# Optimization experiments

Hardware: AMD Instinct MI355X
Metric: run time of the kernel (lower is better)

## Reference

```python
import jax, jax.numpy as jnp
import numpy as np

B, S = 256, 2048
VOCAB, E, H, OUT = 10, 32, 64, 10


def setup_inputs() -> dict:
    key = jax.random.key(0)
    ks = jax.random.split(key, 8)
    num1 = jax.random.randint(ks[0], (B, S), 0, VOCAB, dtype=jnp.int32)
    num2 = jax.random.randint(ks[1], (B, S), 0, VOCAB, dtype=jnp.int32)
    embed = jax.random.normal(ks[2], (VOCAB, E), dtype=jnp.float32) * 0.05
    Wx = jax.random.normal(ks[3], (2 * E, H), dtype=jnp.float32) * (1.0 / np.sqrt(2 * E))
    Wh = jax.random.normal(ks[4], (H, H), dtype=jnp.float32) * (1.0 / np.sqrt(H))
    b = jnp.zeros((H,), dtype=jnp.float32)
    Wd = jax.random.normal(ks[5], (H, OUT), dtype=jnp.float32) * (1.0 / np.sqrt(H))
    bd = jnp.zeros((OUT,), dtype=jnp.float32)
    return {"num1": num1, "num2": num2, "embed": embed, "Wx": Wx,
            "Wh": Wh, "b": b, "Wd": Wd, "bd": bd}


def reference(num1, num2, embed, Wx, Wh, b, Wd, bd):
    # embedding lookup + concat -> [B, S, 2E]
    x = jnp.concatenate([embed[num1], embed[num2]], axis=2)
    # precompute input projection once (big GEMM), scan only the recurrence
    xw = jnp.einsum('bse,eh->bsh', x, Wx) + b  # [B, S, H]

    def step(h, xw_t):
        h = jnp.tanh(xw_t + h @ Wh)  # SimpleRNNCell: tanh(x W + h U + b)
        return h, h

    h0 = jnp.zeros((x.shape[0], Wh.shape[0]), dtype=x.dtype)
    _, hs = jax.lax.scan(step, h0, jnp.swapaxes(xw, 0, 1))  # hs: [S, B, H]
    hs = jnp.swapaxes(hs, 0, 1)  # [B, S, H]
    logits = jnp.einsum('bsh,ho->bso', hs, Wd) + bd  # [B, S, 10]
    return logits
```

## Files before the change

kernel.cpp:

```cpp
#include <hip/hip_runtime.h>

namespace {
typedef float v2f __attribute__((ext_vector_type(2)));
constexpr int kB = 256;
constexpr int kS = 2048;
constexpr int kV = 10;
constexpr int kE = 32;
constexpr int kH = 64;
constexpr int kO = 10;
constexpr int kT = 16;
constexpr int kPad = 68;
constexpr int kTiles = kS / kT;
constexpr float kC = 2.885390081777927f;

__device__ __forceinline__ float step_tanh(float s) {
    s = __builtin_amdgcn_fmed3f(s, -26.f, 26.f);
    float e = __builtin_amdgcn_exp2f(s);
    float r = __builtin_amdgcn_rcpf(e + 1.f);
    return fmaf(-2.f, r, 1.f);
}

__device__ __forceinline__ void do_logits(const float* __restrict__ hb,
                                          const float (* __restrict__ WdT)[kPad],
                                          const float* __restrict__ bdL,
                                          float* __restrict__ out, int obase, int l)
{
    #pragma unroll
    for (int r = 0; r < 3; ++r) {
        int f = r * 64 + l;
        if (f < kT * kO) {
            int tl = f / kO;
            int o  = f - tl * kO;
            const float4* hb4 = reinterpret_cast<const float4*>(hb + tl * kPad);
            const float4* wd4 = reinterpret_cast<const float4*>(&WdT[o][0]);
            float a0 = bdL[o], a1 = 0.f, a2 = 0.f, a3 = 0.f;
            #pragma unroll
            for (int c = 0; c < kH / 4; ++c) {
                float4 h4 = hb4[c];
                float4 w4 = wd4[c];
                a0 = fmaf(h4.x, w4.x, a0);
                a1 = fmaf(h4.y, w4.y, a1);
                a2 = fmaf(h4.z, w4.z, a2);
                a3 = fmaf(h4.w, w4.w, a3);
            }
            out[obase + f] = (a0 + a1) + (a2 + a3);
        }
    }
}

__global__ __launch_bounds__(128, 1)
void rnn_fused(const int* __restrict__ num1, const int* __restrict__ num2,
               const float* __restrict__ embed, const float* __restrict__ Wx,
               const float* __restrict__ Wh, const float* __restrict__ bias,
               const float* __restrict__ Wd, const float* __restrict__ bd,
               float* __restrict__ out)
{
    const int row = blockIdx.x;
    const int tid = threadIdx.x;
    const int w   = tid >> 6;
    const int l   = tid & 63;

    __shared__ __align__(16) float TT[kV * kV][kH];
    __shared__ __align__(16) float hbuf[2][kT][kPad];
    __shared__ __align__(16) float WdT[kO][kPad];
    __shared__ float bdL[kO];

    v2f whc2[kH / 2];
    float h = 0.f;
    int idx_next = 0;
    const int lane16 = l & 15;
    const int nb = row * kS;
    const int orow = row * (kS * kO);

    if (w == 0) {
        float wxc[2 * kE];
        #pragma unroll
        for (int k = 0; k < 2 * kE; ++k) wxc[k] = Wx[k * kH + l];
        float bj = bias[l];
        float t1[kV], t2[kV];
        #pragma unroll
        for (int v = 0; v < kV; ++v) {
            float a0 = 0.f, a1 = 0.f;
            #pragma unroll
            for (int k = 0; k < kE; ++k) {
                float e = embed[v * kE + k];
                a0 = fmaf(e, wxc[k], a0);
                a1 = fmaf(e, wxc[kE + k], a1);
            }
            t1[v] = a0; t2[v] = a1;
        }
        #pragma unroll
        for (int v1 = 0; v1 < kV; ++v1)
            #pragma unroll
            for (int v2 = 0; v2 < kV; ++v2)
                TT[v1 * kV + v2][l] = kC * (t1[v1] + t2[v2] + bj);
        #pragma unroll
        for (int i = 0; i < kH / 2; ++i) {
            v2f t;
            t.x = kC * Wh[(2 * i)     * kH + l];
            t.y = kC * Wh[(2 * i + 1) * kH + l];
            whc2[i] = t;
        }
        hbuf[1][kT - 1][l] = 0.f;
        idx_next = num1[nb + lane16] * kV + num2[nb + lane16];
        __builtin_amdgcn_s_setprio(1);
    } else {
        #pragma unroll
        for (int o = 0; o < kO; ++o) WdT[o][l] = Wd[l * kO + o];
        if (l < kO) bdL[l] = bd[l];
    }
    __syncthreads();

    const float* prevRow = &hbuf[1][kT - 1][0];

    for (int ti = 0; ti < kTiles; ++ti) {
        if (w == 0) {
            const int idxv = idx_next;
            if (ti + 1 < kTiles) {
                int tt = nb + (ti + 1) * kT + lane16;
                idx_next = num1[tt] * kV + num2[tt];
            }
            float* curBase = &hbuf[ti & 1][0][0];
            #pragma unroll 1
            for (int tl = 0; tl < kT; ++tl) {
                const int sidx = __builtin_amdgcn_readlane(idxv, tl);
                const float xwv = TT[sidx][l];
                const float4* hq = reinterpret_cast<const float4*>(prevRow);
                float4 q[16];
                #pragma unroll
                for (int c = 0; c < 16; ++c) q[c] = hq[c];
                __builtin_amdgcn_sched_barrier(0);
                v2f pl[4], ph[4];
                #pragma unroll
                for (int i = 0; i < 4; ++i) { pl[i] = (v2f){0.f, 0.f};
                                              ph[i] = (v2f){0.f, 0.f}; }
                #pragma unroll
                for (int c = 0; c < 16; ++c) {
                    v2f lo; lo.x = q[c].x; lo.y = q[c].y;
                    v2f hi; hi.x = q[c].z; hi.y = q[c].w;
                    pl[c & 3] = lo * whc2[2 * c]     + pl[c & 3];
                    ph[c & 3] = hi * whc2[2 * c + 1] + ph[c & 3];
                }
                v2f t = ((pl[0] + pl[1]) + (pl[2] + pl[3]))
                      + ((ph[0] + ph[1]) + (ph[2] + ph[3]));
                h = step_tanh((t.x + t.y) + xwv);
                float* wr = curBase + tl * kPad;
                wr[l] = h;
                prevRow = wr;
            }
        } else if (ti > 0) {
            do_logits(&hbuf[(ti - 1) & 1][0][0], WdT, bdL, out,
                      orow + (ti - 1) * kT * kO, l);
        }
        __syncthreads();
    }
    if (w == 1)
        do_logits(&hbuf[(kTiles - 1) & 1][0][0], WdT, bdL, out,
                  orow + (kS - kT) * kO, l);
}
}

extern "C" void kernel_launch(void* const* d_in, const int* in_sizes, int n_in,
                              void* d_out, int out_size, void* d_ws, size_t ws_size,
                              hipStream_t stream) {
    (void)in_sizes; (void)n_in; (void)d_ws; (void)ws_size; (void)out_size;
    rnn_fused<<<dim3(kB), dim3(128), 0, stream>>>(
        (const int*)d_in[0], (const int*)d_in[1],
        (const float*)d_in[2], (const float*)d_in[3],
        (const float*)d_in[4], (const float*)d_in[5],
        (const float*)d_in[6], (const float*)d_in[7],
        (float*)d_out);
}
```

Baseline: 492.8 us.

## Process two batch rows per block with split-K matvec and lane shuffle exchange

Each block now runs the recurrences for two batch rows and the grid is halved. Each lane reads half of the previous hidden state for each row and computes partial sums for its own column and its partner column (lane ^ 32). The two halves are combined with a cross-lane shuffle before the tanh. The aim is to interleave two independent recurrence chains so LDS and FMA latency overlap, at the cost of an extra shuffle on the serial path, twice the per-wave FMA work, and only 128 blocks on a 256-CU device.

```diff
diff --git a/kernel.cpp b/kernel.cpp
--- a/kernel.cpp
+++ b/kernel.cpp
@@ -48,6 +48,16 @@
     }
 }
 
+#define ACQ(Q, c, O0, O1, P0, P1)                                           \
+    do {                                                                    \
+        v2f lo_; lo_.x = (Q).x; lo_.y = (Q).y;                              \
+        v2f hi_; hi_.x = (Q).z; hi_.y = (Q).w;                              \
+        O0 = lo_ * whcA2[2 * (c)]     + O0;                                 \
+        O1 = hi_ * whcA2[2 * (c) + 1] + O1;                                 \
+        P0 = lo_ * whcB2[2 * (c)]     + P0;                                 \
+        P1 = hi_ * whcB2[2 * (c) + 1] + P1;                                 \
+    } while (0)
+
 __global__ __launch_bounds__(128, 1)
 void rnn_fused(const int* __restrict__ num1, const int* __restrict__ num2,
                const float* __restrict__ embed, const float* __restrict__ Wx,
@@ -55,22 +65,25 @@
                const float* __restrict__ Wd, const float* __restrict__ bd,
                float* __restrict__ out)
 {
-    const int row = blockIdx.x;
+    const int rowA = blockIdx.x * 2;
+    const int rowB = rowA + 1;
     const int tid = threadIdx.x;
     const int w   = tid >> 6;
     const int l   = tid & 63;
+    const int lx  = l ^ 32;
+    const int kbase = (l >> 5) * 32;
 
     __shared__ __align__(16) float TT[kV * kV][kH];
-    __shared__ __align__(16) float hbuf[2][kT][kPad];
+    __shared__ __align__(16) float hbufA[2][kT][kPad];
+    __shared__ __align__(16) float hbufB[2][kT][kPad];
     __shared__ __align__(16) float WdT[kO][kPad];
     __shared__ float bdL[kO];
 
-    v2f whc2[kH / 2];
-    float h = 0.f;
-    int idx_next = 0;
+    v2f whcA2[kH / 4], whcB2[kH / 4];
+    int idxA_next = 0, idxB_next = 0;
     const int lane16 = l & 15;
-    const int nb = row * kS;
-    const int orow = row * (kS * kO);
+    const int nbA = rowA * kS, nbB = rowB * kS;
+    const int orowA = rowA * (kS * kO), orowB = rowB * (kS * kO);
 
     if (w == 0) {
         float wxc[2 * kE];
@@ -95,14 +108,18 @@
             for (int v2 = 0; v2 < kV; ++v2)
                 TT[v1 * kV + v2][l] = kC * (t1[v1] + t2[v2] + bj);
         #pragma unroll
-        for (int i = 0; i < kH / 2; ++i) {
-            v2f t;
-            t.x = kC * Wh[(2 * i)     * kH + l];
-            t.y = kC * Wh[(2 * i + 1) * kH + l];
-            whc2[i] = t;
-        }
-        hbuf[1][kT - 1][l] = 0.f;
-        idx_next = num1[nb + lane16] * kV + num2[nb + lane16];
+        for (int i = 0; i < kH / 4; ++i) {
+            v2f ta, tb;
+            ta.x = kC * Wh[(kbase + 2 * i)     * kH + l];
+            ta.y = kC * Wh[(kbase + 2 * i + 1) * kH + l];
+            tb.x = kC * Wh[(kbase + 2 * i)     * kH + lx];
+            tb.y = kC * Wh[(kbase + 2 * i + 1) * kH + lx];
+            whcA2[i] = ta; whcB2[i] = tb;
+        }
+        hbufA[1][kT - 1][l] = 0.f;
+        hbufB[1][kT - 1][l] = 0.f;
+        idxA_next = num1[nbA + lane16] * kV + num2[nbA + lane16];
+        idxB_next = num1[nbB + lane16] * kV + num2[nbB + lane16];
         __builtin_amdgcn_s_setprio(1);
     } else {
         #pragma unroll
@@ -111,60 +128,81 @@
     }
     __syncthreads();
 
-    const float* prevRow = &hbuf[1][kT - 1][0];
+    const float* prevA = &hbufA[1][kT - 1][0];
+    const float* prevB = &hbufB[1][kT - 1][0];
 
     for (int ti = 0; ti < kTiles; ++ti) {
         if (w == 0) {
-            const int idxv = idx_next;
+            const int idxvA = idxA_next, idxvB = idxB_next;
             if (ti + 1 < kTiles) {
-                int tt = nb + (ti + 1) * kT + lane16;
-                idx_next = num1[tt] * kV + num2[tt];
-            }
-            float* curBase = &hbuf[ti & 1][0][0];
+                int ta = nbA + (ti + 1) * kT + lane16;
+                int tb = nbB + (ti + 1) * kT + lane16;
+                idxA_next = num1[ta] * kV + num2[ta];
+                idxB_next = num1[tb] * kV + num2[tb];
+            }
+            float* curA = &hbufA[ti & 1][0][0];
+            float* curB = &hbufB[ti & 1][0][0];
             #pragma unroll 1
             for (int tl = 0; tl < kT; ++tl) {
-                const int sidx = __builtin_amdgcn_readlane(idxv, tl);
-                const float xwv = TT[sidx][l];
-                const float4* hq = reinterpret_cast<const float4*>(prevRow);
-                float4 q[16];
-                #pragma unroll
-                for (int c = 0; c < 16; ++c) q[c] = hq[c];
+                const int sA = __builtin_amdgcn_readlane(idxvA, tl);
+                const int sB = __builtin_amdgcn_readlane(idxvB, tl);
+                const float xwA = TT[sA][l];
+                const float xwB = TT[sB][l];
+                const float4* hqA = reinterpret_cast<const float4*>(prevA + kbase);
+                const float4* hqB = reinterpret_cast<const float4*>(prevB + kbase);
+                float4 A0 = hqA[0], A1 = hqA[1], A2 = hqA[2], A3 = hqA[3];
+                float4 A4 = hqA[4], A5 = hqA[5], A6 = hqA[6], A7 = hqA[7];
+                float4 B0 = hqB[0], B1 = hqB[1], B2 = hqB[2], B3 = hqB[3];
+                float4 B4 = hqB[4], B5 = hqB[5], B6 = hqB[6], B7 = hqB[7];
                 __builtin_amdgcn_sched_barrier(0);
-                v2f pl[4], ph[4];
-                #pragma unroll
-                for (int i = 0; i < 4; ++i) { pl[i] = (v2f){0.f, 0.f};
-                                              ph[i] = (v2f){0.f, 0.f}; }
-                #pragma unroll
-                for (int c = 0; c < 16; ++c) {
-                    v2f lo; lo.x = q[c].x; lo.y = q[c].y;
-                    v2f hi; hi.x = q[c].z; hi.y = q[c].w;
-                    pl[c & 3] = lo * whc2[2 * c]     + pl[c & 3];
-                    ph[c & 3] = hi * whc2[2 * c + 1] + ph[c & 3];
-                }
-                v2f t = ((pl[0] + pl[1]) + (pl[2] + pl[3]))
-                      + ((ph[0] + ph[1]) + (ph[2] + ph[3]));
-                h = step_tanh((t.x + t.y) + xwv);
-                float* wr = curBase + tl * kPad;
-                wr[l] = h;
-                prevRow = wr;
+                v2f Ao0; Ao0.x = xwA; Ao0.y = 0.f;
+                v2f Ao1 = {0.f, 0.f}, Ap0 = {0.f, 0.f}, Ap1 = {0.f, 0.f};
+                v2f Bo0; Bo0.x = xwB; Bo0.y = 0.f;
+                v2f Bo1 = {0.f, 0.f}, Bp0 = {0.f, 0.f}, Bp1 = {0.f, 0.f};
+                ACQ(A0, 0, Ao0, Ao1, Ap0, Ap1); ACQ(A1, 1, Ao0, Ao1, Ap0, Ap1);
+                ACQ(A2, 2, Ao0, Ao1, Ap0, Ap1); ACQ(A3, 3, Ao0, Ao1, Ap0, Ap1);
+                ACQ(A4, 4, Ao0, Ao1, Ap0, Ap1); ACQ(A5, 5, Ao0, Ao1, Ap0, Ap1);
+                ACQ(A6, 6, Ao0, Ao1, Ap0, Ap1); ACQ(A7, 7, Ao0, Ao1, Ap0, Ap1);
+                ACQ(B0, 0, Bo0, Bo1, Bp0, Bp1); ACQ(B1, 1, Bo0, Bo1, Bp0, Bp1);
+                ACQ(B2, 2, Bo0, Bo1, Bp0, Bp1); ACQ(B3, 3, Bo0, Bo1, Bp0, Bp1);
+                ACQ(B4, 4, Bo0, Bo1, Bp0, Bp1); ACQ(B5, 5, Bo0, Bo1, Bp0, Bp1);
+                ACQ(B6, 6, Bo0, Bo1, Bp0, Bp1); ACQ(B7, 7, Bo0, Bo1, Bp0, Bp1);
+                v2f Apv = Ap0 + Ap1;  float pParA = Apv.x + Apv.y;
+                v2f Bpv = Bp0 + Bp1;  float pParB = Bpv.x + Bpv.y;
+                float othA = __shfl(pParA, lx, 64);
+                float othB = __shfl(pParB, lx, 64);
+                v2f Aov = Ao0 + Ao1;  float pOwnA = Aov.x + Aov.y;
+                v2f Bov = Bo0 + Bo1;  float pOwnB = Bov.x + Bov.y;
+                float hA = step_tanh(pOwnA + othA);
+                float* wrA = curA + tl * kPad;
+                wrA[l] = hA;  prevA = wrA;
+                float hB = step_tanh(pOwnB + othB);
+                float* wrB = curB + tl * kPad;
+                wrB[l] = hB;  prevB = wrB;
             }
         } else if (ti > 0) {
-            do_logits(&hbuf[(ti - 1) & 1][0][0], WdT, bdL, out,
-                      orow + (ti - 1) * kT * kO, l);
+            do_logits(&hbufA[(ti - 1) & 1][0][0], WdT, bdL, out,
+                      orowA + (ti - 1) * kT * kO, l);
+            do_logits(&hbufB[(ti - 1) & 1][0][0], WdT, bdL, out,
+                      orowB + (ti - 1) * kT * kO, l);
         }
         __syncthreads();
     }
-    if (w == 1)
-        do_logits(&hbuf[(kTiles - 1) & 1][0][0], WdT, bdL, out,
-                  orow + (kS - kT) * kO, l);
-}
+    if (w == 1) {
+        do_logits(&hbufA[(kTiles - 1) & 1][0][0], WdT, bdL, out,
+                  orowA + (kS - kT) * kO, l);
+        do_logits(&hbufB[(kTiles - 1) & 1][0][0], WdT, bdL, out,
+                  orowB + (kS - kT) * kO, l);
+    }
+}
+#undef ACQ
 }
 
 extern "C" void kernel_launch(void* const* d_in, const int* in_sizes, int n_in,
                               void* d_out, int out_size, void* d_ws, size_t ws_size,
                               hipStream_t stream) {
     (void)in_sizes; (void)n_in; (void)d_ws; (void)ws_size; (void)out_size;
-    rnn_fused<<<dim3(kB), dim3(128), 0, stream>>>(
+    rnn_fused<<<dim3(kB / 2), dim3(128), 0, stream>>>(
         (const int*)d_in[0], (const int*)d_in[1],
         (const float*)d_in[2], (const float*)d_in[3],
         (const float*)d_in[4], (const float*)d_in[5],
```

New measurement: 910.4 us. 84.7% more time.

## Split recurrence dot product across half-waves and exchange partials with permlane32 swap

Applied to the files above, without the earlier changes.

Each lane now reads only half of the previous hidden state (32 values instead of 64) and computes partial sums for both its own output column and its partner lane's column (l^32). The partner's partial is exchanged with permlane32_swap and added to the lane's own partial. The aim is to halve the LDS reads per step on the serial recurrence's critical path and shorten the dependent accumulation chains. In exchange it adds a cross-lane swap, a different FMA summation order, and fewer independent accumulators.

```diff
diff --git a/kernel.cpp b/kernel.cpp
--- a/kernel.cpp
+++ b/kernel.cpp
@@ -2,6 +2,7 @@
 
 namespace {
 typedef float v2f __attribute__((ext_vector_type(2)));
+typedef unsigned u32x2 __attribute__((ext_vector_type(2)));
 constexpr int kB = 256;
 constexpr int kS = 2048;
 constexpr int kV = 10;
@@ -18,6 +19,13 @@
     float e = __builtin_amdgcn_exp2f(s);
     float r = __builtin_amdgcn_rcpf(e + 1.f);
     return fmaf(-2.f, r, 1.f);
+}
+
+__device__ __forceinline__ float swap32(float p) {
+    u32x2 r = __builtin_amdgcn_permlane32_swap(__float_as_uint(p),
+                                               __float_as_uint(p),
+                                               false, false);
+    return (__uint_as_float(r.x) + __uint_as_float(r.y)) - p;
 }
 
 __device__ __forceinline__ void do_logits(const float* __restrict__ hb,
@@ -59,14 +67,15 @@
     const int tid = threadIdx.x;
     const int w   = tid >> 6;
     const int l   = tid & 63;
+    const int lx  = l ^ 32;
+    const int kbase = (l >> 5) * 32;
 
     __shared__ __align__(16) float TT[kV * kV][kH];
     __shared__ __align__(16) float hbuf[2][kT][kPad];
     __shared__ __align__(16) float WdT[kO][kPad];
     __shared__ float bdL[kO];
 
-    v2f whc2[kH / 2];
-    float h = 0.f;
+    v2f whcA2[kH / 4], whcB2[kH / 4];
     int idx_next = 0;
     const int lane16 = l & 15;
     const int nb = row * kS;
@@ -95,11 +104,13 @@
             for (int v2 = 0; v2 < kV; ++v2)
                 TT[v1 * kV + v2][l] = kC * (t1[v1] + t2[v2] + bj);
         #pragma unroll
-        for (int i = 0; i < kH / 2; ++i) {
-            v2f t;
-            t.x = kC * Wh[(2 * i)     * kH + l];
-            t.y = kC * Wh[(2 * i + 1) * kH + l];
-            whc2[i] = t;
+        for (int i = 0; i < kH / 4; ++i) {
+            v2f ta, tb;
+            ta.x = kC * Wh[(kbase + 2 * i)     * kH + l];
+            ta.y = kC * Wh[(kbase + 2 * i + 1) * kH + l];
+            tb.x = kC * Wh[(kbase + 2 * i)     * kH + lx];
+            tb.y = kC * Wh[(kbase + 2 * i + 1) * kH + lx];
+            whcA2[i] = ta; whcB2[i] = tb;
         }
         hbuf[1][kT - 1][l] = 0.f;
         idx_next = num1[nb + lane16] * kV + num2[nb + lane16];
@@ -125,27 +136,28 @@
             for (int tl = 0; tl < kT; ++tl) {
                 const int sidx = __builtin_amdgcn_readlane(idxv, tl);
                 const float xwv = TT[sidx][l];
-                const float4* hq = reinterpret_cast<const float4*>(prevRow);
-                float4 q[16];
+                const float4* hq = reinterpret_cast<const float4*>(prevRow + kbase);
+                float4 q[8];
                 #pragma unroll
-                for (int c = 0; c < 16; ++c) q[c] = hq[c];
+                for (int c = 0; c < 8; ++c) q[c] = hq[c];
                 __builtin_amdgcn_sched_barrier(0);
-                v2f pl[4], ph[4];
+                v2f o0; o0.x = xwv; o0.y = 0.f;
+                v2f o1 = {0.f, 0.f}, r0 = {0.f, 0.f}, r1 = {0.f, 0.f};
                 #pragma unroll
-                for (int i = 0; i < 4; ++i) { pl[i] = (v2f){0.f, 0.f};
-                                              ph[i] = (v2f){0.f, 0.f}; }
-                #pragma unroll
-                for (int c = 0; c < 16; ++c) {
+                for (int c = 0; c < 8; ++c) {
                     v2f lo; lo.x = q[c].x; lo.y = q[c].y;
                     v2f hi; hi.x = q[c].z; hi.y = q[c].w;
-                    pl[c & 3] = lo * whc2[2 * c]     + pl[c & 3];
-                    ph[c & 3] = hi * whc2[2 * c + 1] + ph[c & 3];
+                    o0 = lo * whcA2[2 * c]     + o0;
+                    o1 = hi * whcA2[2 * c + 1] + o1;
+                    r0 = lo * whcB2[2 * c]     + r0;
+                    r1 = hi * whcB2[2 * c + 1] + r1;
                 }
-                v2f t = ((pl[0] + pl[1]) + (pl[2] + pl[3]))
-                      + ((ph[0] + ph[1]) + (ph[2] + ph[3]));
-                h = step_tanh((t.x + t.y) + xwv);
+                v2f rv = r0 + r1;  float pPar = rv.x + rv.y;
+                float oth = swap32(pPar);
+                v2f ov = o0 + o1;  float pOwn = ov.x + ov.y;
+                float hcur = step_tanh(pOwn + oth);
                 float* wr = curBase + tl * kPad;
-                wr[l] = h;
+                wr[l] = hcur;
                 prevRow = wr;
             }
         } else if (ti > 0) {
```

New measurement: 456.2 us. 1.08x faster.
